# Optimization experiments

Measured on AMD Instinct MI355X. Metric: run time of the kernel, lower is better.

The kernel has to match this reference:

```python
import jax, jax.numpy as jnp
import numpy as np

N_EMBD = 1024
B, T = 4, 2048

def setup_inputs() -> dict:
    key = jax.random.key(0)
    k1, k2, k3, k4 = jax.random.split(key, 4)
    s = 1.0 / np.sqrt(N_EMBD)
    return {
        "x": jax.random.normal(k1, (B, T, N_EMBD), dtype=jnp.float32),
        "Wq": jax.random.normal(k2, (N_EMBD, N_EMBD), dtype=jnp.float32) * s,
        "Wk": jax.random.normal(k3, (N_EMBD, N_EMBD), dtype=jnp.float32) * s,
        "Wv": jax.random.normal(k4, (N_EMBD, N_EMBD), dtype=jnp.float32) * s,
    }

def reference(x, Wq, Wk, Wv):
    # x: [B,T,C]; torch Linear (no bias): y = x @ W.T
    Bq, Tq, C = x.shape
    q = jnp.einsum('btc,dc->btd', x, Wq)
    k = jnp.einsum('btc,dc->btd', x, Wk)
    v = jnp.einsum('btc,dc->btd', x, Wv)
    att = jnp.einsum('bqd,bkd->bqk', q, k) / jnp.sqrt(jnp.float32(C))
    causal = jnp.tril(jnp.ones((Tq, Tq), dtype=bool))  # [T,T]
    att = jnp.where(causal, att, -jnp.inf)
    w = jax.nn.softmax(att, axis=-1)
    # dropout is identity in eval mode
    out = jnp.einsum('bqk,bkd->bqd', w, v)
    return out
```

## Files before the change

### kernel.cpp

```cpp
#include <hip/hip_runtime.h>
#include <stdint.h>

typedef __attribute__((ext_vector_type(8))) __bf16 bf16x8;
typedef __attribute__((ext_vector_type(8))) unsigned short ushort8;
typedef __attribute__((ext_vector_type(4))) float f32x4;

static __device__ __forceinline__ unsigned short f2bf(float f) {
  unsigned u = __float_as_uint(f);
  u += 0x7fffu + ((u >> 16) & 1u);
  return (unsigned short)(u >> 16);
}

union U16cast { ushort8 u; bf16x8 b; };
static __device__ __forceinline__ bf16x8 as_bf16x8(ushort8 x) { U16cast t; t.u = x; return t.b; }
static __device__ __forceinline__ bf16x8 ldfrag(const unsigned short* p) {
  return as_bf16x8(*(const ushort8*)p);
}

#define GLD_LDS16(g, l)                                                        \
  __builtin_amdgcn_global_load_lds(                                            \
      (const __attribute__((address_space(1))) void*)(g),                      \
      (__attribute__((address_space(3))) void*)(l), 16, 0, 0)

__global__ __launch_bounds__(256) void cast_all(
    const float* __restrict__ x, const float* __restrict__ Wq,
    const float* __restrict__ Wk, const float* __restrict__ Wv,
    unsigned short* __restrict__ out, float* __restrict__ lzero,
    long nx4, long nw4, long n4) {
  long g = (long)blockIdx.x * blockDim.x + threadIdx.x;
  if (g < 2048) ((float4*)lzero)[g] = (float4){0.f, 0.f, 0.f, 0.f};
  long i = g;
  long stride = (long)gridDim.x * blockDim.x;
  for (; i < n4; i += stride) {
    const float4* src;
    long j = i;
    if (j < nx4) {
      src = (const float4*)x;
    } else {
      j -= nx4;
      if (j < nw4) src = (const float4*)Wq;
      else if (j < 2 * nw4) { src = (const float4*)Wk; j -= nw4; }
      else { src = (const float4*)Wv; j -= 2 * nw4; }
    }
    float4 v = src[j];
    ushort4 o;
    o.x = f2bf(v.x); o.y = f2bf(v.y); o.z = f2bf(v.z); o.w = f2bf(v.w);
    *(ushort4*)(out + i * 4) = o;
  }
}

__global__ __launch_bounds__(512, 4) void gemm_qkv(
    const unsigned short* __restrict__ A, const unsigned short* __restrict__ B,
    unsigned short* __restrict__ qkv, unsigned short* __restrict__ vT) {
  __shared__ __align__(16) unsigned short As[2][4096];
  __shared__ __align__(16) unsigned short Bs[2][8192];

  int wg = blockIdx.x;
  wg = (wg & 7) * 96 + (wg >> 3);
  const int bm = wg / 12, bn = wg % 12;
  const int m0 = bm << 7, n0 = bn << 8;

  const int tid = threadIdx.x;

  const int srow = tid >> 2;
  const int sseg = (tid & 3) ^ ((srow >> 1) & 3);
  const unsigned short* sa = A + (long)(m0 + srow) * 1024 + sseg * 8;
  const unsigned short* sb0 = B + (long)(n0 + srow) * 1024 + sseg * 8;
  const unsigned short* sb1 = sb0 + (long)128 * 1024;
  unsigned short* dA = &As[0][0] + tid * 8;
  unsigned short* dB = &Bs[0][0] + tid * 8;

#define STG(kt, s)                                                             \
  do {                                                                         \
    GLD_LDS16(sa + (kt) * 32, dA + (s) * 4096);                                \
    GLD_LDS16(sb0 + (kt) * 32, dB + (s) * 8192);                               \
    GLD_LDS16(sb1 + (kt) * 32, dB + (s) * 8192 + 4096);                        \
  } while (0)

  const int lane = tid & 63;
  const int w = tid >> 6;
  const int wr = w >> 2;
  const int wc = w & 3;
  const int fr = lane & 15;
  const int kb = lane >> 4;
  const int segr = (kb ^ ((fr >> 1) & 3)) << 3;
  const unsigned short* rA = &As[0][0] + (wr * 64 + fr) * 32 + segr;
  const unsigned short* rB = &Bs[0][0] + (wc * 64 + fr) * 32 + segr;

  f32x4 acc[4][4];
#pragma unroll
  for (int mf = 0; mf < 4; ++mf)
#pragma unroll
    for (int nf = 0; nf < 4; ++nf)
      acc[mf][nf] = (f32x4){0.f, 0.f, 0.f, 0.f};

  STG(0, 0);
  __syncthreads();

  for (int kt = 0; kt < 32; ++kt) {
    const int s = kt & 1;
    if (kt + 1 < 32) STG(kt + 1, s ^ 1);

    const unsigned short* pA = rA + s * 4096;
    const unsigned short* pB = rB + s * 8192;
    bf16x8 av[4], bv[4];
#pragma unroll
    for (int mf = 0; mf < 4; ++mf) av[mf] = ldfrag(pA + mf * 512);
#pragma unroll
    for (int nf = 0; nf < 4; ++nf) bv[nf] = ldfrag(pB + nf * 512);

#pragma unroll
    for (int mf = 0; mf < 4; ++mf)
#pragma unroll
      for (int nf = 0; nf < 4; ++nf)
        acc[mf][nf] = __builtin_amdgcn_mfma_f32_16x16x32_bf16(av[mf], bv[nf], acc[mf][nf], 0, 0, 0);

    __syncthreads();
  }
#undef STG

  const int rq = kb << 2;
  if (n0 < 2048) {
#pragma unroll
    for (int mf = 0; mf < 4; ++mf) {
      const int row = m0 + wr * 64 + mf * 16 + rq;
#pragma unroll
      for (int nf = 0; nf < 4; ++nf) {
        const int col = n0 + wc * 64 + nf * 16 + fr;
#pragma unroll
        for (int r = 0; r < 4; ++r)
          qkv[(long)(row + r) * 3072 + col] = f2bf(acc[mf][nf][r]);
      }
    }
  } else {
    const int b2 = m0 >> 11;
    const int t0 = (m0 & 2047) + wr * 64;
#pragma unroll
    for (int mf = 0; mf < 4; ++mf) {
      const int trow = t0 + mf * 16 + rq;
#pragma unroll
      for (int nf = 0; nf < 4; ++nf) {
        const int colv = (n0 - 2048) + wc * 64 + nf * 16 + fr;
        ushort4 o;
        o.x = f2bf(acc[mf][nf][0]); o.y = f2bf(acc[mf][nf][1]);
        o.z = f2bf(acc[mf][nf][2]); o.w = f2bf(acc[mf][nf][3]);
        *(ushort4*)(vT + ((long)b2 * 1024 + colv) * 2048 + trow) = o;
      }
    }
  }
}

template <int MODE>
__global__ __launch_bounds__(256, 4) void gemm128(
    const unsigned short* __restrict__ A, const unsigned short* __restrict__ Bp,
    void* __restrict__ Cout, float* __restrict__ lbuf) {
  __shared__ __align__(16) unsigned short As[2][4096];
  __shared__ __align__(16) unsigned short Bs[2][4096];

  constexpr int LDA = (MODE == 1) ? 3072 : 2048;

  const int wgid = blockIdx.x;
  int m0, n0, b;
  if constexpr (MODE == 1) {
    b = wgid & 3;
    const int t = wgid >> 2;
    int bm = 0;
    while ((bm + 2) * (bm + 1) / 2 <= t) ++bm;
    const int bn = t - bm * (bm + 1) / 2;
    m0 = bm << 7; n0 = bn << 7;
  } else {
    const int xcd = wgid & 7;
    const int inner = wgid >> 3;
    const int s = inner >> 5;
    const int rem = inner & 31;
    b = rem >> 3;
    const int bn = rem & 7;
    const int bm = s ? (15 - xcd) : xcd;
    m0 = bm << 7; n0 = bn << 7;
  }

  const unsigned short* Ab = A;
  const unsigned short* Bb = Bp;
  if constexpr (MODE == 1) {
    Ab += (long)b * 2048 * 3072;
    Bb += (long)b * 2048 * 3072;
  } else {
    Ab += (long)b * 2048 * 2048;
    Bb += (long)b * 1024 * 2048;
  }

  const int tid = threadIdx.x;

  const int srow = tid >> 2;
  const int sseg = (tid & 3) ^ ((srow >> 1) & 3);
  const unsigned short* sa = Ab + (long)(m0 + srow) * LDA + sseg * 8;
  const unsigned short* sb = Bb + (long)(n0 + srow) * LDA + sseg * 8;
  const long sRj = (long)64 * LDA;
  unsigned short* dA = &As[0][0] + tid * 8;
  unsigned short* dB = &Bs[0][0] + tid * 8;

#define STG(kt, s)                                                             \
  do {                                                                         \
    GLD_LDS16(sa + (kt) * 32, dA + (s) * 4096);                                \
    GLD_LDS16(sa + sRj + (kt) * 32, dA + (s) * 4096 + 2048);                   \
    GLD_LDS16(sb + (kt) * 32, dB + (s) * 4096);                                \
    GLD_LDS16(sb + sRj + (kt) * 32, dB + (s) * 4096 + 2048);                   \
  } while (0)

  const int lane = tid & 63;
  const int w = tid >> 6;
  const int wr = w >> 1;
  const int wc = w & 1;
  const int fr = lane & 15;
  const int kb = lane >> 4;
  const unsigned short* rA0 = &As[0][0] + wr * 64 * 32;
  const unsigned short* rB0 = &Bs[0][0] + wc * 64 * 32;

  const int rq = kb << 2;

  float il[4][4];
  if constexpr (MODE == 2) {
    const float* lrow = lbuf + b * 2048;
#pragma unroll
    for (int mf = 0; mf < 4; ++mf) {
      const int row = m0 + wr * 64 + mf * 16 + rq;
#pragma unroll
      for (int r = 0; r < 4; ++r) il[mf][r] = 1.0f / lrow[row + r];
    }
  }

  f32x4 acc[4][4];
#pragma unroll
  for (int mf = 0; mf < 4; ++mf)
#pragma unroll
    for (int nf = 0; nf < 4; ++nf)
      acc[mf][nf] = (f32x4){0.f, 0.f, 0.f, 0.f};

  const int kend = (MODE == 2) ? (m0 + 128) : 1024;
  const int NT = kend >> 5;

  STG(0, 0);
  __syncthreads();

  for (int kt = 0; kt < NT; ++kt) {
    const int s = kt & 1;
    if (kt + 1 < NT) STG(kt + 1, s ^ 1);

    bf16x8 av[4], bvv[4];
#pragma unroll
    for (int mf = 0; mf < 4; ++mf) {
      const int row = mf * 16 + fr;
      const int segr = (kb ^ ((row >> 1) & 3)) << 3;
      av[mf] = ldfrag(rA0 + s * 4096 + row * 32 + segr);
    }
#pragma unroll
    for (int nf = 0; nf < 4; ++nf) {
      const int row = nf * 16 + fr;
      const int segr = (kb ^ ((row >> 1) & 3)) << 3;
      bvv[nf] = ldfrag(rB0 + s * 4096 + row * 32 + segr);
    }

#pragma unroll
    for (int mf = 0; mf < 4; ++mf)
#pragma unroll
      for (int nf = 0; nf < 4; ++nf)
        acc[mf][nf] = __builtin_amdgcn_mfma_f32_16x16x32_bf16(av[mf], bvv[nf], acc[mf][nf], 0, 0, 0);

    __syncthreads();
  }
#undef STG

  if constexpr (MODE == 1) {
    unsigned short* Pu = (unsigned short*)Cout + (long)b * 2048 * 2048;
    float* lrow = lbuf + b * 2048;
#pragma unroll
    for (int mf = 0; mf < 4; ++mf) {
      const int row = m0 + wr * 64 + mf * 16 + rq;
      float psum0 = 0.f, psum1 = 0.f, psum2 = 0.f, psum3 = 0.f;
#pragma unroll
      for (int nf = 0; nf < 4; ++nf) {
        const int col = n0 + wc * 64 + nf * 16 + fr;
        float e0 = (col > row + 0) ? 0.f : __expf(acc[mf][nf][0] * 0.03125f);
        float e1 = (col > row + 1) ? 0.f : __expf(acc[mf][nf][1] * 0.03125f);
        float e2 = (col > row + 2) ? 0.f : __expf(acc[mf][nf][2] * 0.03125f);
        float e3 = (col > row + 3) ? 0.f : __expf(acc[mf][nf][3] * 0.03125f);
        psum0 += e0; psum1 += e1; psum2 += e2; psum3 += e3;
        Pu[(long)(row + 0) * 2048 + col] = f2bf(e0);
        Pu[(long)(row + 1) * 2048 + col] = f2bf(e1);
        Pu[(long)(row + 2) * 2048 + col] = f2bf(e2);
        Pu[(long)(row + 3) * 2048 + col] = f2bf(e3);
      }
#pragma unroll
      for (int off = 1; off < 16; off <<= 1) {
        psum0 += __shfl_xor(psum0, off);
        psum1 += __shfl_xor(psum1, off);
        psum2 += __shfl_xor(psum2, off);
        psum3 += __shfl_xor(psum3, off);
      }
      if (fr == 0) {
        atomicAdd(&lrow[row + 0], psum0);
        atomicAdd(&lrow[row + 1], psum1);
        atomicAdd(&lrow[row + 2], psum2);
        atomicAdd(&lrow[row + 3], psum3);
      }
    }
  } else {
    float* Cf = (float*)Cout + (long)b * 2048 * 1024;
#pragma unroll
    for (int mf = 0; mf < 4; ++mf) {
      const int row = m0 + wr * 64 + mf * 16 + rq;
#pragma unroll
      for (int nf = 0; nf < 4; ++nf) {
        const int col = n0 + wc * 64 + nf * 16 + fr;
        Cf[(long)(row + 0) * 1024 + col] = acc[mf][nf][0] * il[mf][0];
        Cf[(long)(row + 1) * 1024 + col] = acc[mf][nf][1] * il[mf][1];
        Cf[(long)(row + 2) * 1024 + col] = acc[mf][nf][2] * il[mf][2];
        Cf[(long)(row + 3) * 1024 + col] = acc[mf][nf][3] * il[mf][3];
      }
    }
  }
}

extern "C" void kernel_launch(void* const* d_in, const int* in_sizes, int n_in,
                              void* d_out, int out_size, void* d_ws, size_t ws_size,
                              hipStream_t stream) {
  const float* x  = (const float*)d_in[0];
  const float* Wq = (const float*)d_in[1];
  const float* Wk = (const float*)d_in[2];
  const float* Wv = (const float*)d_in[3];
  float* out = (float*)d_out;

  const int Bb = 4, T = 2048, C = 1024;
  const long BT = (long)Bb * T;
  const int N3 = 3 * C;

  char* ws = (char*)d_ws;
  unsigned short* xb   = (unsigned short*)ws; ws += BT * C * 2;
  unsigned short* wbuf = (unsigned short*)ws; ws += (long)N3 * C * 2;
  unsigned short* qkv  = (unsigned short*)ws; ws += BT * N3 * 2;
  unsigned short* vT   = (unsigned short*)ws; ws += BT * C * 2;
  unsigned short* Pu   = (unsigned short*)ws; ws += (long)Bb * T * T * 2;
  float* lbuf          = (float*)ws;          ws += BT * 4;

  const long nx4 = BT * C / 4, nw4 = (long)C * C / 4;
  cast_all<<<2048, 256, 0, stream>>>(x, Wq, Wk, Wv, xb, lbuf, nx4, nw4, nx4 + 3 * nw4);

  gemm_qkv<<<dim3(768, 1, 1), 512, 0, stream>>>(xb, wbuf, qkv, vT);

  gemm128<1><<<dim3(544, 1, 1), 256, 0, stream>>>(qkv, qkv + C, Pu, lbuf);

  gemm128<2><<<dim3(512, 1, 1), 256, 0, stream>>>(Pu, vT, out, lbuf);
}
```

Measured before the change: 156.0 us.

## Enlarge QKV GEMM tile to 256x384 with 8x6 MFMA fragments per wave

The QKV projection GEMM tile grows from 128x256 to 256x384, so the grid shrinks from 768 to 256 workgroups and each wave computes a 128x96 sub-tile. The aim is more reuse of each LDS fragment load per MFMA and less global/LDS staging traffic per output element. In exchange, register pressure rises (48 accumulator vectors), LDS use grows, and occupancy drops to 2 blocks per CU. With 256 workgroups the grid may also fill the device's compute units poorly, and the epilogue now chooses between the qkv and transposed-V stores per fragment.

```diff
diff --git a/kernel.cpp b/kernel.cpp
--- a/kernel.cpp
+++ b/kernel.cpp
@@ -49,49 +49,51 @@
   }
 }
 
-__global__ __launch_bounds__(512, 4) void gemm_qkv(
+__global__ __launch_bounds__(512, 2) void gemm_qkv(
     const unsigned short* __restrict__ A, const unsigned short* __restrict__ B,
     unsigned short* __restrict__ qkv, unsigned short* __restrict__ vT) {
-  __shared__ __align__(16) unsigned short As[2][4096];
-  __shared__ __align__(16) unsigned short Bs[2][8192];
+  __shared__ __align__(16) unsigned short As[2][8192];
+  __shared__ __align__(16) unsigned short Bs[2][12288];
 
   int wg = blockIdx.x;
-  wg = (wg & 7) * 96 + (wg >> 3);
-  const int bm = wg / 12, bn = wg % 12;
-  const int m0 = bm << 7, n0 = bn << 8;
+  wg = (wg & 7) * 32 + (wg >> 3);
+  const int bm = wg >> 3, bn = wg & 7;
+  const int m0 = bm << 8;
+  const int n0 = bn * 384;
 
   const int tid = threadIdx.x;
 
   const int srow = tid >> 2;
   const int sseg = (tid & 3) ^ ((srow >> 1) & 3);
   const unsigned short* sa = A + (long)(m0 + srow) * 1024 + sseg * 8;
-  const unsigned short* sb0 = B + (long)(n0 + srow) * 1024 + sseg * 8;
-  const unsigned short* sb1 = sb0 + (long)128 * 1024;
+  const unsigned short* sb = B + (long)(n0 + srow) * 1024 + sseg * 8;
   unsigned short* dA = &As[0][0] + tid * 8;
   unsigned short* dB = &Bs[0][0] + tid * 8;
 
 #define STG(kt, s)                                                             \
   do {                                                                         \
-    GLD_LDS16(sa + (kt) * 32, dA + (s) * 4096);                                \
-    GLD_LDS16(sb0 + (kt) * 32, dB + (s) * 8192);                               \
-    GLD_LDS16(sb1 + (kt) * 32, dB + (s) * 8192 + 4096);                        \
+    GLD_LDS16(sa + (kt) * 32, dA + (s) * 8192);                                \
+    GLD_LDS16(sa + 131072 + (kt) * 32, dA + (s) * 8192 + 4096);                \
+    GLD_LDS16(sb + (kt) * 32, dB + (s) * 12288);                               \
+    GLD_LDS16(sb + 131072 + (kt) * 32, dB + (s) * 12288 + 4096);               \
+    GLD_LDS16(sb + 262144 + (kt) * 32, dB + (s) * 12288 + 8192);               \
   } while (0)
 
   const int lane = tid & 63;
   const int w = tid >> 6;
-  const int wr = w >> 2;
-  const int wc = w & 3;
+  const int wrm = w >> 2;
+  const int wcn = w & 3;
   const int fr = lane & 15;
   const int kb = lane >> 4;
   const int segr = (kb ^ ((fr >> 1) & 3)) << 3;
-  const unsigned short* rA = &As[0][0] + (wr * 64 + fr) * 32 + segr;
-  const unsigned short* rB = &Bs[0][0] + (wc * 64 + fr) * 32 + segr;
-
-  f32x4 acc[4][4];
-#pragma unroll
-  for (int mf = 0; mf < 4; ++mf)
-#pragma unroll
-    for (int nf = 0; nf < 4; ++nf)
+  const unsigned short* rA = &As[0][0] + (wrm * 128 + fr) * 32 + segr;
+  const unsigned short* rB = &Bs[0][0] + (wcn * 96 + fr) * 32 + segr;
+
+  f32x4 acc[8][6];
+#pragma unroll
+  for (int mf = 0; mf < 8; ++mf)
+#pragma unroll
+    for (int nf = 0; nf < 6; ++nf)
       acc[mf][nf] = (f32x4){0.f, 0.f, 0.f, 0.f};
 
   STG(0, 0);
@@ -101,46 +103,41 @@
     const int s = kt & 1;
     if (kt + 1 < 32) STG(kt + 1, s ^ 1);
 
-    const unsigned short* pA = rA + s * 4096;
-    const unsigned short* pB = rB + s * 8192;
-    bf16x8 av[4], bv[4];
-#pragma unroll
-    for (int mf = 0; mf < 4; ++mf) av[mf] = ldfrag(pA + mf * 512);
-#pragma unroll
-    for (int nf = 0; nf < 4; ++nf) bv[nf] = ldfrag(pB + nf * 512);
-
-#pragma unroll
-    for (int mf = 0; mf < 4; ++mf)
-#pragma unroll
-      for (int nf = 0; nf < 4; ++nf)
-        acc[mf][nf] = __builtin_amdgcn_mfma_f32_16x16x32_bf16(av[mf], bv[nf], acc[mf][nf], 0, 0, 0);
+    const unsigned short* pA = rA + s * 8192;
+    const unsigned short* pB = rB + s * 12288;
+
+    bf16x8 bv[6];
+#pragma unroll
+    for (int nf = 0; nf < 6; ++nf) bv[nf] = ldfrag(pB + nf * 512);
+
+#pragma unroll
+    for (int mf = 0; mf < 8; ++mf) {
+      bf16x8 av = ldfrag(pA + mf * 512);
+#pragma unroll
+      for (int nf = 0; nf < 6; ++nf)
+        acc[mf][nf] = __builtin_amdgcn_mfma_f32_16x16x32_bf16(av, bv[nf], acc[mf][nf], 0, 0, 0);
+    }
 
     __syncthreads();
   }
 #undef STG
 
   const int rq = kb << 2;
-  if (n0 < 2048) {
-#pragma unroll
-    for (int mf = 0; mf < 4; ++mf) {
-      const int row = m0 + wr * 64 + mf * 16 + rq;
-#pragma unroll
-      for (int nf = 0; nf < 4; ++nf) {
-        const int col = n0 + wc * 64 + nf * 16 + fr;
+#pragma unroll
+  for (int mf = 0; mf < 8; ++mf) {
+    const int row = m0 + wrm * 128 + mf * 16 + rq;
+#pragma unroll
+    for (int nf = 0; nf < 6; ++nf) {
+      const int colb = n0 + wcn * 96 + nf * 16;
+      if (colb < 2048) {
+        const int col = colb + fr;
 #pragma unroll
         for (int r = 0; r < 4; ++r)
           qkv[(long)(row + r) * 3072 + col] = f2bf(acc[mf][nf][r]);
-      }
-    }
-  } else {
-    const int b2 = m0 >> 11;
-    const int t0 = (m0 & 2047) + wr * 64;
-#pragma unroll
-    for (int mf = 0; mf < 4; ++mf) {
-      const int trow = t0 + mf * 16 + rq;
-#pragma unroll
-      for (int nf = 0; nf < 4; ++nf) {
-        const int colv = (n0 - 2048) + wc * 64 + nf * 16 + fr;
+      } else {
+        const int b2 = m0 >> 11;
+        const int trow = (m0 & 2047) + wrm * 128 + mf * 16 + rq;
+        const int colv = colb - 2048 + fr;
         ushort4 o;
         o.x = f2bf(acc[mf][nf][0]); o.y = f2bf(acc[mf][nf][1]);
         o.z = f2bf(acc[mf][nf][2]); o.w = f2bf(acc[mf][nf][3]);
@@ -345,7 +342,7 @@
   const long nx4 = BT * C / 4, nw4 = (long)C * C / 4;
   cast_all<<<2048, 256, 0, stream>>>(x, Wq, Wk, Wv, xb, lbuf, nx4, nw4, nx4 + 3 * nw4);
 
-  gemm_qkv<<<dim3(768, 1, 1), 512, 0, stream>>>(xb, wbuf, qkv, vT);
+  gemm_qkv<<<dim3(256, 1, 1), 512, 0, stream>>>(xb, wbuf, qkv, vT);
 
   gemm128<1><<<dim3(544, 1, 1), 256, 0, stream>>>(qkv, qkv + C, Pu, lbuf);
 
```

Result: no change. 153.5 us (-1.6%).
